# Optimization experiments

Measured on AMD Instinct MI355X. Metric: run time of the kernel, lower is better.

## Reference

```python
import jax, jax.numpy as jnp
import numpy as np

DELTA = 1e-6
B, INPUT, N, WL, R = 32, 1024, 1024, 64, 4
IFACE = WL * R + 3 * WL + 5 * R + 3  # 471


def setup_inputs() -> dict:
    key = jax.random.key(0)
    ks = jax.random.split(key, 9)
    return {
        "x": jax.random.normal(ks[0], (B, INPUT), jnp.float32),
        "W_if": jax.random.normal(ks[1], (INPUT, IFACE), jnp.float32) * 0.02,
        "b_if": jnp.zeros((IFACE,), jnp.float32),
        "memory": jax.random.normal(ks[2], (B, N, WL), jnp.float32) * 0.1,
        "link_matrix": jax.random.uniform(ks[3], (B, 1, N, N), jnp.float32) * 1e-3,
        "precedence": jax.random.uniform(ks[4], (B, 1, N), jnp.float32) * 1e-2,
        "read_weights": jax.random.uniform(ks[5], (B, R, N), jnp.float32) / N,
        "write_weights": jax.random.uniform(ks[6], (B, 1, N), jnp.float32) / N,
        "usage": jax.random.uniform(ks[7], (B, N), jnp.float32),
    }


def _content(memory, keys, strengths):
    # cosine-similarity content addressing; memory [b,N,W], keys [b,h,W]
    mn = memory / (jnp.linalg.norm(memory, axis=-1, keepdims=True) + DELTA)
    kn = keys / (jnp.linalg.norm(keys, axis=-1, keepdims=True) + DELTA)
    sim = jnp.einsum('bhw,bnw->bhn', kn, mn)
    return jax.nn.softmax(sim * strengths[..., None], axis=-1)


def reference(x, W_if, b_if, memory, link_matrix, precedence, read_weights, write_weights, usage):
    b = x.shape[0]
    xi = x @ W_if + b_if  # [b, IFACE]

    # --- parse interface vector (offsets per the torch module) ---
    o = 0
    read_keys = jnp.tanh(xi[:, o:o + R * WL].reshape(b, R, WL)); o += R * WL
    read_strengths = jax.nn.softplus(xi[:, o:o + R]); o += R            # [b,r]
    write_key = jnp.tanh(xi[:, o:o + WL].reshape(b, 1, WL)); o += WL
    write_strength = jax.nn.softplus(xi[:, o:o + 1]); o += 1            # [b,1]
    erase_vector = jax.nn.sigmoid(xi[:, o:o + WL].reshape(b, 1, WL)); o += WL
    write_vector = jnp.tanh(xi[:, o:o + WL].reshape(b, 1, WL)); o += WL
    free_gates = jax.nn.sigmoid(xi[:, o:o + R]); o += R                 # [b,r]
    allocation_gate = jax.nn.sigmoid(xi[:, o:o + 1]); o += 1            # [b,1]
    write_gate = jax.nn.sigmoid(xi[:, o:o + 1]); o += 1                 # [b,1]
    read_modes = jax.nn.softmax(xi[:, o:o + 3 * R].reshape(b, R, 3), axis=-1)

    # --- write phase ---
    wcw = _content(memory, write_key, write_strength)  # [b,1,N]

    # usage update
    u = usage + (1.0 - usage) * (1.0 - jnp.prod(1.0 - write_weights, axis=1))
    psi = jnp.prod(1.0 - free_gates[:, :, None] * read_weights, axis=1)
    u = u * psi

    # allocation via ascending sort + exclusive cumprod, then unsort
    u = DELTA + (1.0 - DELTA) * u
    perm = jnp.argsort(u, axis=1)                       # ascending usage order (phi)
    sorted_u = jnp.take_along_axis(u, perm, axis=1)
    ones_col = jnp.ones((b, 1), u.dtype)
    prod_su = jnp.cumprod(jnp.concatenate([ones_col, sorted_u], axis=1), axis=1)[:, :-1]
    sorted_alloc = (1.0 - sorted_u) * prod_su
    inv_perm = jnp.argsort(perm, axis=1)                # phi_rev: inverse permutation
    alloc = jnp.take_along_axis(sorted_alloc, inv_perm, axis=1)[:, None, :]  # [b,1,N]

    # write weighting
    ag = allocation_gate[..., None]
    wg = write_gate[..., None]
    ww = wg * (ag * alloc + (1.0 - ag) * wcw)           # [b,1,N]

    # memory erase + write (h = 1 write head)
    new_memory = memory * (1.0 - jnp.einsum('bhn,bhw->bnw', ww, erase_vector)) \
                 + jnp.einsum('bhn,bhw->bnw', ww, write_vector)

    # link matrix update (NxN outer-product, zero diagonal)
    ww_i = ww[:, :, :, None]                            # [b,1,N,1]
    ww_j = ww[:, :, None, :]                            # [b,1,1,N]
    prec_j = precedence[:, :, None, :]                  # [b,1,1,N]
    new_link = (1.0 - ww_i - ww_j) * link_matrix + ww_i * prec_j
    eye_mask = 1.0 - jnp.eye(N, dtype=new_link.dtype)
    new_link = new_link * eye_mask[None, None, :, :]

    # precedence update
    new_prec = (1.0 - jnp.sum(ww, axis=-1, keepdims=True)) * precedence + ww

    # --- read phase ---
    fwd_w = jnp.einsum('bhij,brj->bri', new_link, read_weights)   # forward links
    bwd_w = jnp.einsum('bhji,brj->bri', new_link, read_weights)   # backward links
    crw = _content(new_memory, read_keys, read_strengths)         # [b,r,N]
    new_rw = read_modes[..., 0:1] * bwd_w + read_modes[..., 1:2] * crw + read_modes[..., 2:3] * fwd_w
    read_vectors = jnp.einsum('brn,bnw->brw', new_rw, new_memory)  # [b,r,W]
    return read_vectors
```

## Files before the change

### kernel.cpp

```cpp
#include <hip/hip_runtime.h>
#include <math.h>

#define DELTA_ 1e-6f
#define IFACE_ 471
#define XI_STRIDE 480

#define OFF_XI    0
#define OFF_RKN   15360
#define OFF_RS    23552
#define OFF_ER    23680
#define OFF_WV    25728
#define OFF_RM    27776
#define OFF_WW    28160
#define OFF_WWRW  60928
#define OFF_PRD   192000
#define OFF_WRD   192128
#define OFF_INVN  192256
#define OFF_DIAG  225024
#define OFF_NM    257792
#define OFF_RA    2354944
#define OFF_RB    2486016
#define OFF_SAP   2617088
#define OFF_SBP   4714240

__device__ __forceinline__ float sigm_(float x){ return 1.f/(1.f+expf(-x)); }
__device__ __forceinline__ float softp_(float x){ return fmaxf(x,0.f)+log1pf(expf(-fabsf(x))); }
__device__ __forceinline__ float dot4_(float4 a, float4 b){ return a.x*b.x+a.y*b.y+a.z*b.z+a.w*b.w; }

__global__ __launch_bounds__(256) void k_xi(const float* __restrict__ x,
    const float* __restrict__ W, const float* __restrict__ bias,
    float* __restrict__ xi) {
  int b = blockIdx.x;
  int j0 = blockIdx.y*64;
  int t = threadIdx.x;
  int jl = t & 63, kq = t >> 6;
  __shared__ __align__(16) float sx[1024];
  __shared__ float s_part[256];
  for (int q=t; q<256; q+=256) ((float4*)sx)[q] = ((const float4*)(x + b*1024))[q];
  __syncthreads();
  int j = j0 + jl;
  int jc = j < IFACE_ ? j : IFACE_-1;
  float acc = 0.f;
  const float* Wp = W + (size_t)kq*256*IFACE_ + jc;
  #pragma unroll 4
  for (int k=0;k<256;++k) acc += sx[kq*256+k]*Wp[(size_t)k*IFACE_];
  s_part[t] = acc;
  __syncthreads();
  if (t < 64 && (j0+t) < IFACE_) {
    xi[b*XI_STRIDE + j0+t] = s_part[t]+s_part[64+t]+s_part[128+t]+s_part[192+t] + bias[j0+t];
  }
}

__global__ __launch_bounds__(256) void k_batch(
    const float* __restrict__ xi, const float* __restrict__ memory,
    const float* __restrict__ usage, const float* __restrict__ read_w,
    const float* __restrict__ write_w, const float* __restrict__ precedence,
    float* __restrict__ rkn, float* __restrict__ rs, float* __restrict__ er,
    float* __restrict__ wv, float* __restrict__ rm, float* __restrict__ ww_out,
    float* __restrict__ wwrw, float* __restrict__ prd, float* __restrict__ wrd) {
  int b = blockIdx.x; int t = threadIdx.x;
  int lane = t & 63; int wave = t >> 6;
  __shared__ float s_act[472];
  __shared__ __align__(16) float s_key[64];
  __shared__ float s_wcw[1024];
  __shared__ unsigned long long s_k64[1024];
  __shared__ float s_ps[1024];
  __shared__ float s_alloc[1024];
  __shared__ float s_red[32];
  __shared__ float s_bc[2];

  for (int q = t; q < IFACE_; q += 256) {
    float v = xi[b*XI_STRIDE+q];
    float a;
    if      (q < 256) a = tanhf(v);
    else if (q < 260) a = softp_(v);
    else if (q < 324) a = tanhf(v);
    else if (q < 325) a = softp_(v);
    else if (q < 389) a = sigm_(v);
    else if (q < 453) a = tanhf(v);
    else if (q < 459) a = sigm_(v);
    else              a = v;
    s_act[q] = a;
  }
  __syncthreads();
  if (t < 4) {
    float m0=s_act[459+3*t], m1=s_act[460+3*t], m2=s_act[461+3*t];
    float mx=fmaxf(m0,fmaxf(m1,m2));
    float e0=expf(m0-mx), e1=expf(m1-mx), e2=expf(m2-mx);
    float s=e0+e1+e2;
    rm[b*12+3*t+0]=e0/s; rm[b*12+3*t+1]=e1/s; rm[b*12+3*t+2]=e2/s;
  }
  if (t < 64) { er[b*64+t]=s_act[325+t]; wv[b*64+t]=s_act[389+t]; }
  {
    int r = wave;
    float v = s_act[r*64+lane];
    float ss = v*v;
    for (int off=32; off; off>>=1) ss += __shfl_xor(ss, off);
    rkn[((size_t)b*4+r)*64+lane] = v / (sqrtf(ss)+DELTA_);
    if (lane==0) rs[b*4+r] = s_act[256+r];
  }
  if (wave==0) {
    float v = s_act[260+lane];
    float ss=v*v;
    for (int off=32; off; off>>=1) ss += __shfl_xor(ss, off);
    s_key[lane] = v/(sqrtf(ss)+DELTA_);
  }
  __syncthreads();
  float wstr = s_act[324], agv = s_act[457], wgv = s_act[458];

  for (int n=t; n<1024; n+=256) {
    const float4* row = (const float4*)(memory + ((size_t)b*1024+n)*64);
    float dot=0.f, nn2=0.f;
    #pragma unroll
    for (int w4=0; w4<16; ++w4) {
      float4 m4 = row[w4];
      float4 k4 = ((const float4*)s_key)[w4];
      dot += dot4_(m4,k4);
      nn2 += dot4_(m4,m4);
    }
    s_wcw[n] = dot/(sqrtf(nn2)+DELTA_) * wstr;
  }
  __syncthreads();
  {
    float lm=-1e30f;
    for (int n=t;n<1024;n+=256) lm=fmaxf(lm,s_wcw[n]);
    for (int off=32;off;off>>=1) lm=fmaxf(lm,__shfl_xor(lm,off));
    if (lane==0) s_red[wave]=lm;
    __syncthreads();
    if (t==0) s_bc[0]=fmaxf(fmaxf(s_red[0],s_red[1]),fmaxf(s_red[2],s_red[3]));
    __syncthreads();
    float mx=s_bc[0], ls=0.f;
    for (int n=t;n<1024;n+=256){ float e=expf(s_wcw[n]-mx); s_wcw[n]=e; ls+=e; }
    for (int off=32;off;off>>=1) ls+=__shfl_xor(ls,off);
    if (lane==0) s_red[wave]=ls;
    __syncthreads();
    if (t==0) s_bc[1]=s_red[0]+s_red[1]+s_red[2]+s_red[3];
    __syncthreads();
    float inv=1.f/s_bc[1];
    for (int n=t;n<1024;n+=256) s_wcw[n]*=inv;
  }
  __syncthreads();

  for (int n=t; n<1024; n+=256) {
    float us = usage[b*1024+n];
    float wwi = write_w[b*1024+n];
    float u = us + (1.f-us)*wwi;
    float psi = 1.f;
    #pragma unroll
    for (int r=0;r<4;++r) psi *= (1.f - s_act[453+r]*read_w[((size_t)b*4+r)*1024+n]);
    u *= psi;
    u = DELTA_ + (1.f-DELTA_)*u;
    unsigned int ub = __float_as_uint(u);
    s_k64[n] = ((unsigned long long)ub<<32) | (unsigned int)n;
  }

  for (int k=2; k<=1024; k<<=1) {
    for (int j=k>>1; j>0; j>>=1) {
      __syncthreads();
      for (int idx=t; idx<1024; idx+=256) {
        int partner = idx ^ j;
        if (partner > idx) {
          unsigned long long a=s_k64[idx], c=s_k64[partner];
          bool asc = ((idx & k) == 0);
          bool sw = asc ? (a > c) : (a < c);
          if (sw) { s_k64[idx]=c; s_k64[partner]=a; }
        }
      }
    }
  }
  __syncthreads();

  for (int n=t;n<1024;n+=256) s_ps[n] = __uint_as_float((unsigned int)(s_k64[n]>>32));
  __syncthreads();
  for (int off=1; off<1024; off<<=1) {
    float tmp[4];
    #pragma unroll
    for (int m=0;m<4;++m){ int n=t+256*m; tmp[m] = (n>=off)? s_ps[n-off] : 1.f; }
    __syncthreads();
    #pragma unroll
    for (int m=0;m<4;++m){ int n=t+256*m; s_ps[n] *= tmp[m]; }
    __syncthreads();
  }
  for (int n=t;n<1024;n+=256) {
    unsigned long long kv = s_k64[n];
    float su = __uint_as_float((unsigned int)(kv>>32));
    int oi = (int)(kv & 0xffffffffu);
    float prod = (n==0)?1.f:s_ps[n-1];
    s_alloc[oi] = (1.f-su)*prod;
  }
  __syncthreads();

  float pp[4]={0,0,0,0}, wp[4]={0,0,0,0};
  for (int n=t;n<1024;n+=256) {
    float w_ = wgv*(agv*s_alloc[n] + (1.f-agv)*s_wcw[n]);
    ww_out[b*1024+n]=w_;
    float pn = precedence[b*1024+n];
    #pragma unroll
    for (int r=0;r<4;++r){
      float rwv = read_w[((size_t)b*4+r)*1024+n];
      wwrw[((size_t)b*4+r)*1024+n] = w_*rwv;
      pp[r] += pn*rwv;
      wp[r] += w_*rwv;
    }
  }
  #pragma unroll
  for (int r=0;r<4;++r){
    for (int off=32;off;off>>=1){ pp[r]+=__shfl_xor(pp[r],off); wp[r]+=__shfl_xor(wp[r],off); }
  }
  if (lane==0){
    #pragma unroll
    for (int r=0;r<4;++r){ s_red[wave*8+r]=pp[r]; s_red[wave*8+4+r]=wp[r]; }
  }
  __syncthreads();
  if (t<4)              prd[b*4+t]   = s_red[t]+s_red[8+t]+s_red[16+t]+s_red[24+t];
  else if (t<8){ int r=t-4; wrd[b*4+r] = s_red[4+r]+s_red[12+r]+s_red[20+r]+s_red[28+r]; }
}

__global__ __launch_bounds__(256) void k_newmem(const float* __restrict__ memory,
    const float* __restrict__ ww, const float* __restrict__ er,
    const float* __restrict__ wv, float* __restrict__ newmem, float* __restrict__ invn) {
  int b = blockIdx.x;
  int n0 = blockIdx.y*64;
  int t = threadIdx.x;
  int lane16 = t & 15, rl = t >> 4;
  __shared__ float s_ww[64];
  __shared__ __align__(16) float s_er[64];
  __shared__ __align__(16) float s_wv[64];
  if (t < 64) s_ww[t] = ww[b*1024 + n0 + t];
  else if (t < 128) s_er[t-64] = er[b*64 + (t-64)];
  else if (t < 192) s_wv[t-128] = wv[b*64 + (t-128)];
  __syncthreads();
  float4 e4 = ((const float4*)s_er)[lane16];
  float4 v4 = ((const float4*)s_wv)[lane16];
  #pragma unroll
  for (int p=0;p<4;++p) {
    int rloc = p*16 + rl;
    int row = n0 + rloc;
    float wn = s_ww[rloc];
    size_t i4 = ((size_t)b*1024+row)*16 + lane16;
    float4 m4 = ((const float4*)memory)[i4];
    float4 nv;
    nv.x = m4.x*(1.f-wn*e4.x) + wn*v4.x;
    nv.y = m4.y*(1.f-wn*e4.y) + wn*v4.y;
    nv.z = m4.z*(1.f-wn*e4.z) + wn*v4.z;
    nv.w = m4.w*(1.f-wn*e4.w) + wn*v4.w;
    ((float4*)newmem)[i4] = nv;
    float ss = dot4_(nv,nv);
    ss += __shfl_xor(ss,1); ss += __shfl_xor(ss,2);
    ss += __shfl_xor(ss,4); ss += __shfl_xor(ss,8);
    if (lane16==0) invn[b*1024+row] = 1.f/(sqrtf(ss)+DELTA_);
  }
}

__global__ __launch_bounds__(256) void k_fwd(const float* __restrict__ L,
    const float* __restrict__ read_w, const float* __restrict__ wwrw,
    float* __restrict__ RA, float* __restrict__ RB) {
  int b = blockIdx.x;
  int i0 = blockIdx.y*64;
  __shared__ __align__(16) float4 s_rw[4][256];
  __shared__ __align__(16) float4 s_wr[4][256];
  for (int q=threadIdx.x; q<1024; q+=256) {
    int r=q>>8, c4=q&255;
    s_rw[r][c4] = ((const float4*)(read_w + ((size_t)b*4+r)*1024))[c4];
    s_wr[r][c4] = ((const float4*)(wwrw   + ((size_t)b*4+r)*1024))[c4];
  }
  __syncthreads();
  int wave=threadIdx.x>>6, lane=threadIdx.x&63;
  for (int qg=0; qg<4; ++qg) {
    int ib = i0 + wave*16 + qg*4;
    const float4* r0 = (const float4*)(L + ((size_t)b*1024 + ib+0)*1024);
    const float4* r1 = (const float4*)(L + ((size_t)b*1024 + ib+1)*1024);
    const float4* r2 = (const float4*)(L + ((size_t)b*1024 + ib+2)*1024);
    const float4* r3 = (const float4*)(L + ((size_t)b*1024 + ib+3)*1024);
    float acc[4][8];
    #pragma unroll
    for (int q=0;q<4;++q) for (int d=0;d<8;++d) acc[q][d]=0.f;
    #pragma unroll
    for (int m=0;m<4;++m){
      int c4 = lane + (m<<6);
      float4 l0=r0[c4], l1=r1[c4], l2=r2[c4], l3=r3[c4];
      #pragma unroll
      for (int r=0;r<4;++r){
        float4 rv=s_rw[r][c4], wv4=s_wr[r][c4];
        acc[0][r]+=dot4_(l0,rv); acc[0][r+4]+=dot4_(l0,wv4);
        acc[1][r]+=dot4_(l1,rv); acc[1][r+4]+=dot4_(l1,wv4);
        acc[2][r]+=dot4_(l2,rv); acc[2][r+4]+=dot4_(l2,wv4);
        acc[3][r]+=dot4_(l3,rv); acc[3][r+4]+=dot4_(l3,wv4);
      }
    }
    #pragma unroll
    for (int q=0;q<4;++q){
      #pragma unroll
      for (int d=0;d<8;++d){
        float v=acc[q][d];
        for (int off=32;off;off>>=1) v+=__shfl_xor(v,off);
        if (lane==0){
          int i = ib+q;
          if (d<4) RA[((size_t)b*4+d)*1024+i]=v;
          else     RB[((size_t)b*4+(d-4))*1024+i]=v;
        }
      }
    }
  }
}

__global__ __launch_bounds__(256) void k_bwd(const float* __restrict__ L,
    const float* __restrict__ read_w, const float* __restrict__ wwrw,
    float* __restrict__ SAp, float* __restrict__ SBp, float* __restrict__ diag) {
  int b = blockIdx.x;
  int rc = blockIdx.y;
  int i0 = rc*64;
  int t = threadIdx.x;
  __shared__ float s_rw[4][64], s_wr[4][64];
  { int r = t>>6, i = t&63;
    s_rw[r][i]=read_w[((size_t)b*4+r)*1024 + i0+i];
    s_wr[r][i]=wwrw  [((size_t)b*4+r)*1024 + i0+i]; }
  __syncthreads();
  float4 sa0={0,0,0,0},sa1={0,0,0,0},sa2={0,0,0,0},sa3={0,0,0,0};
  float4 sb0={0,0,0,0},sb1={0,0,0,0},sb2={0,0,0,0},sb3={0,0,0,0};
  const float4* Lb = (const float4*)(L + (size_t)b*1048576 + (size_t)i0*1024);
  #pragma unroll 4
  for (int i=0;i<64;++i) {
    float4 lv = Lb[(size_t)i*256 + t];
    float w0=s_rw[0][i], w1=s_rw[1][i], w2=s_rw[2][i], w3=s_rw[3][i];
    float u0=s_wr[0][i], u1=s_wr[1][i], u2=s_wr[2][i], u3=s_wr[3][i];
    sa0.x+=lv.x*w0; sa0.y+=lv.y*w0; sa0.z+=lv.z*w0; sa0.w+=lv.w*w0;
    sa1.x+=lv.x*w1; sa1.y+=lv.y*w1; sa1.z+=lv.z*w1; sa1.w+=lv.w*w1;
    sa2.x+=lv.x*w2; sa2.y+=lv.y*w2; sa2.z+=lv.z*w2; sa2.w+=lv.w*w2;
    sa3.x+=lv.x*w3; sa3.y+=lv.y*w3; sa3.z+=lv.z*w3; sa3.w+=lv.w*w3;
    sb0.x+=lv.x*u0; sb0.y+=lv.y*u0; sb0.z+=lv.z*u0; sb0.w+=lv.w*u0;
    sb1.x+=lv.x*u1; sb1.y+=lv.y*u1; sb1.z+=lv.z*u1; sb1.w+=lv.w*u1;
    sb2.x+=lv.x*u2; sb2.y+=lv.y*u2; sb2.z+=lv.z*u2; sb2.w+=lv.w*u2;
    sb3.x+=lv.x*u3; sb3.y+=lv.y*u3; sb3.z+=lv.z*u3; sb3.w+=lv.w*u3;
    int idx = i0 + i;
    if ((idx>>2) == t) {
      int c = idx & 3;
      float d = (c==0)?lv.x:((c==1)?lv.y:((c==2)?lv.z:lv.w));
      diag[b*1024+idx] = d;
    }
  }
  size_t base = (((size_t)(b*16+rc))*4)*1024;
  ((float4*)(SAp + base          ))[t] = sa0;
  ((float4*)(SAp + base + 1024   ))[t] = sa1;
  ((float4*)(SAp + base + 2048   ))[t] = sa2;
  ((float4*)(SAp + base + 3072   ))[t] = sa3;
  ((float4*)(SBp + base          ))[t] = sb0;
  ((float4*)(SBp + base + 1024   ))[t] = sb1;
  ((float4*)(SBp + base + 2048   ))[t] = sb2;
  ((float4*)(SBp + base + 3072   ))[t] = sb3;
}

__global__ __launch_bounds__(256) void k_read(
    const float* __restrict__ newmem, const float* __restrict__ invn,
    const float* __restrict__ rkn, const float* __restrict__ rs,
    const float* __restrict__ rm, const float* __restrict__ RA,
    const float* __restrict__ RB, const float* __restrict__ SAp,
    const float* __restrict__ SBp, const float* __restrict__ ww,
    const float* __restrict__ precedence, const float* __restrict__ read_w,
    const float* __restrict__ diag, const float* __restrict__ prd,
    const float* __restrict__ wrd, float* __restrict__ out) {
  int b=blockIdx.x, r=blockIdx.y;
  int t=threadIdx.x, lane=t&63, wave=t>>6;
  int lane16 = t & 15, rl = t >> 4;
  __shared__ __align__(16) float s_key[64];
  __shared__ float s_arr[1024];
  __shared__ float s_red[4];
  __shared__ float s_bc[2];
  __shared__ __align__(16) float4 s_acc[16][16];
  if (t<64) s_key[t]=rkn[((size_t)b*4+r)*64+t];
  __syncthreads();
  float rstr = rs[b*4+r];
  float4 key4 = ((const float4*)s_key)[lane16];
  for (int p=0;p<64;++p) {
    int row = p*16 + rl;
    float4 m4 = ((const float4*)newmem)[((size_t)b*1024+row)*16 + lane16];
    float d = dot4_(m4, key4);
    d += __shfl_xor(d,1); d += __shfl_xor(d,2);
    d += __shfl_xor(d,4); d += __shfl_xor(d,8);
    if (lane16==0) s_arr[row] = d * invn[b*1024+row] * rstr;
  }
  __syncthreads();
  {
    float lm=-1e30f;
    for (int n=t;n<1024;n+=256) lm=fmaxf(lm,s_arr[n]);
    for (int off=32;off;off>>=1) lm=fmaxf(lm,__shfl_xor(lm,off));
    if (lane==0) s_red[wave]=lm;
    __syncthreads();
    if (t==0) s_bc[0]=fmaxf(fmaxf(s_red[0],s_red[1]),fmaxf(s_red[2],s_red[3]));
    __syncthreads();
    float mx=s_bc[0], ls=0.f;
    for (int n=t;n<1024;n+=256){ float e=expf(s_arr[n]-mx); s_arr[n]=e; ls+=e; }
    for (int off=32;off;off>>=1) ls+=__shfl_xor(ls,off);
    if (lane==0) s_red[wave]=ls;
    __syncthreads();
    if (t==0) s_bc[1]=s_red[0]+s_red[1]+s_red[2]+s_red[3];
    __syncthreads();
    float inv=1.f/s_bc[1];
    for (int n=t;n<1024;n+=256) s_arr[n]*=inv;
  }
  __syncthreads();
  float m0=rm[b*12+r*3+0], m1=rm[b*12+r*3+1], m2=rm[b*12+r*3+2];
  float pd=prd[b*4+r], wd=wrd[b*4+r];
  for (int n=t;n<1024;n+=256) {
    float ra = RA[((size_t)b*4+r)*1024+n];
    float rb = RB[((size_t)b*4+r)*1024+n];
    float sa=0.f, sb=0.f;
    #pragma unroll
    for (int rc=0;rc<16;++rc){
      sa+=SAp[(((size_t)(b*16+rc))*4+r)*1024+n];
      sb+=SBp[(((size_t)(b*16+rc))*4+r)*1024+n];
    }
    float w_ = ww[b*1024+n];
    float pn = precedence[b*1024+n];
    float rwv= read_w[((size_t)b*4+r)*1024+n];
    float dg = diag[b*1024+n];
    float fwd = (1.f-w_)*ra - rb + w_*pd - ((1.f-2.f*w_)*dg + w_*pn)*rwv;
    float bwd = (1.f-w_)*sa - sb + pn*(wd - w_*rwv) - (1.f-2.f*w_)*dg*rwv;
    float crw = s_arr[n];
    __syncthreads();
    s_arr[n] = m0*bwd + m1*crw + m2*fwd;
    __syncthreads();
  }
  __syncthreads();
  float4 acc = {0,0,0,0};
  for (int p=0;p<64;++p) {
    int row = p*16 + rl;
    float4 m4 = ((const float4*)newmem)[((size_t)b*1024+row)*16 + lane16];
    float s = s_arr[row];
    acc.x += s*m4.x; acc.y += s*m4.y; acc.z += s*m4.z; acc.w += s*m4.w;
  }
  s_acc[rl][lane16] = acc;
  __syncthreads();
  if (t < 16) {
    float4 tot = {0,0,0,0};
    #pragma unroll
    for (int g=0; g<16; ++g) {
      float4 v = s_acc[g][t];
      tot.x+=v.x; tot.y+=v.y; tot.z+=v.z; tot.w+=v.w;
    }
    ((float4*)(out + (b*4+r)*64))[t] = tot;
  }
}

extern "C" void kernel_launch(void* const* d_in, const int* in_sizes, int n_in,
                              void* d_out, int out_size, void* d_ws, size_t ws_size,
                              hipStream_t stream) {
  const float* x      = (const float*)d_in[0];
  const float* W_if   = (const float*)d_in[1];
  const float* b_if   = (const float*)d_in[2];
  const float* memory = (const float*)d_in[3];
  const float* link   = (const float*)d_in[4];
  const float* prec   = (const float*)d_in[5];
  const float* read_w = (const float*)d_in[6];
  const float* write_w= (const float*)d_in[7];
  const float* usage  = (const float*)d_in[8];
  float* out = (float*)d_out;
  float* ws = (float*)d_ws;

  float* xi   = ws + OFF_XI;
  float* rkn  = ws + OFF_RKN;
  float* rs   = ws + OFF_RS;
  float* er   = ws + OFF_ER;
  float* wv   = ws + OFF_WV;
  float* rm   = ws + OFF_RM;
  float* wwp  = ws + OFF_WW;
  float* wwrw = ws + OFF_WWRW;
  float* prd  = ws + OFF_PRD;
  float* wrd  = ws + OFF_WRD;
  float* invn = ws + OFF_INVN;
  float* diag = ws + OFF_DIAG;
  float* nm   = ws + OFF_NM;
  float* RA   = ws + OFF_RA;
  float* RB   = ws + OFF_RB;
  float* SAp  = ws + OFF_SAP;
  float* SBp  = ws + OFF_SBP;

  k_xi<<<dim3(32,8), 256, 0, stream>>>(x, W_if, b_if, xi);
  k_batch<<<dim3(32), 256, 0, stream>>>(xi, memory, usage, read_w, write_w, prec,
                                        rkn, rs, er, wv, rm, wwp, wwrw, prd, wrd);
  k_newmem<<<dim3(32,16), 256, 0, stream>>>(memory, wwp, er, wv, nm, invn);
  k_fwd<<<dim3(32,16), 256, 0, stream>>>(link, read_w, wwrw, RA, RB);
  k_bwd<<<dim3(32,16), 256, 0, stream>>>(link, read_w, wwrw, SAp, SBp, diag);
  k_read<<<dim3(32,4), 256, 0, stream>>>(nm, invn, rkn, rs, rm, RA, RB, SAp, SBp,
                                         wwp, prec, read_w, diag, prd, wrd, out);
}
```

Baseline: 393.2 us.

## Fuse forward and backward link-matrix passes into one tiled scan kernel

Merges the separate forward (row-dot) and backward (column-accumulate) passes over the 128MB link matrix into a single kernel. Each 64x256 tile is loaded once and feeds both products, with forward partials written per column chunk and summed later in k_read. This halves the dominant HBM traffic over the link matrix. In exchange it adds per-row wave shuffle reductions, extra shared-memory staging and a larger partial-sum workspace.

New measurement: 411.4 us. 1.05x slower.

```diff
diff --git a/kernel.cpp b/kernel.cpp
--- a/kernel.cpp
+++ b/kernel.cpp
@@ -18,10 +18,10 @@
 #define OFF_INVN  192256
 #define OFF_DIAG  225024
 #define OFF_NM    257792
-#define OFF_RA    2354944
-#define OFF_RB    2486016
-#define OFF_SAP   2617088
-#define OFF_SBP   4714240
+#define OFF_RAP   2354944
+#define OFF_RBP   2879232
+#define OFF_SAP   3403520
+#define OFF_SBP   5500672
 
 __device__ __forceinline__ float sigm_(float x){ return 1.f/(1.f+expf(-x)); }
 __device__ __forceinline__ float softp_(float x){ return fmaxf(x,0.f)+log1pf(expf(-fabsf(x))); }
@@ -252,109 +252,104 @@
   }
 }
 
-__global__ __launch_bounds__(256) void k_fwd(const float* __restrict__ L,
+__global__ __launch_bounds__(256) void k_scan(const float* __restrict__ L,
     const float* __restrict__ read_w, const float* __restrict__ wwrw,
-    float* __restrict__ RA, float* __restrict__ RB) {
-  int b = blockIdx.x;
-  int i0 = blockIdx.y*64;
-  __shared__ __align__(16) float4 s_rw[4][256];
-  __shared__ __align__(16) float4 s_wr[4][256];
-  for (int q=threadIdx.x; q<1024; q+=256) {
-    int r=q>>8, c4=q&255;
-    s_rw[r][c4] = ((const float4*)(read_w + ((size_t)b*4+r)*1024))[c4];
-    s_wr[r][c4] = ((const float4*)(wwrw   + ((size_t)b*4+r)*1024))[c4];
-  }
-  __syncthreads();
-  int wave=threadIdx.x>>6, lane=threadIdx.x&63;
-  for (int qg=0; qg<4; ++qg) {
-    int ib = i0 + wave*16 + qg*4;
-    const float4* r0 = (const float4*)(L + ((size_t)b*1024 + ib+0)*1024);
-    const float4* r1 = (const float4*)(L + ((size_t)b*1024 + ib+1)*1024);
-    const float4* r2 = (const float4*)(L + ((size_t)b*1024 + ib+2)*1024);
-    const float4* r3 = (const float4*)(L + ((size_t)b*1024 + ib+3)*1024);
-    float acc[4][8];
-    #pragma unroll
-    for (int q=0;q<4;++q) for (int d=0;d<8;++d) acc[q][d]=0.f;
-    #pragma unroll
-    for (int m=0;m<4;++m){
-      int c4 = lane + (m<<6);
-      float4 l0=r0[c4], l1=r1[c4], l2=r2[c4], l3=r3[c4];
-      #pragma unroll
-      for (int r=0;r<4;++r){
-        float4 rv=s_rw[r][c4], wv4=s_wr[r][c4];
-        acc[0][r]+=dot4_(l0,rv); acc[0][r+4]+=dot4_(l0,wv4);
-        acc[1][r]+=dot4_(l1,rv); acc[1][r+4]+=dot4_(l1,wv4);
-        acc[2][r]+=dot4_(l2,rv); acc[2][r+4]+=dot4_(l2,wv4);
-        acc[3][r]+=dot4_(l3,rv); acc[3][r+4]+=dot4_(l3,wv4);
-      }
-    }
-    #pragma unroll
-    for (int q=0;q<4;++q){
-      #pragma unroll
-      for (int d=0;d<8;++d){
-        float v=acc[q][d];
-        for (int off=32;off;off>>=1) v+=__shfl_xor(v,off);
-        if (lane==0){
-          int i = ib+q;
-          if (d<4) RA[((size_t)b*4+d)*1024+i]=v;
-          else     RB[((size_t)b*4+(d-4))*1024+i]=v;
-        }
-      }
-    }
-  }
-}
-
-__global__ __launch_bounds__(256) void k_bwd(const float* __restrict__ L,
-    const float* __restrict__ read_w, const float* __restrict__ wwrw,
-    float* __restrict__ SAp, float* __restrict__ SBp, float* __restrict__ diag) {
-  int b = blockIdx.x;
-  int rc = blockIdx.y;
+    float* __restrict__ RAp, float* __restrict__ RBp,
+    float* __restrict__ SAp, float* __restrict__ SBp,
+    float* __restrict__ diag) {
+  int b = blockIdx.x, rc = blockIdx.y, cc = blockIdx.z;
   int i0 = rc*64;
   int t = threadIdx.x;
-  __shared__ float s_rw[4][64], s_wr[4][64];
-  { int r = t>>6, i = t&63;
-    s_rw[r][i]=read_w[((size_t)b*4+r)*1024 + i0+i];
-    s_wr[r][i]=wwrw  [((size_t)b*4+r)*1024 + i0+i]; }
-  __syncthreads();
-  float4 sa0={0,0,0,0},sa1={0,0,0,0},sa2={0,0,0,0},sa3={0,0,0,0};
-  float4 sb0={0,0,0,0},sb1={0,0,0,0},sb2={0,0,0,0},sb3={0,0,0,0};
-  const float4* Lb = (const float4*)(L + (size_t)b*1048576 + (size_t)i0*1024);
+  int tq = t>>6, tl = t&63;
+  __shared__ __align__(16) float smem[4608];
+  {
+    int r = t>>6, idx = t&63;
+    ((float4*)smem)[r*64+idx]        = ((const float4*)(read_w + ((size_t)b*4+r)*1024 + cc*256))[idx];
+    ((float4*)(smem+1024))[r*64+idx] = ((const float4*)(wwrw   + ((size_t)b*4+r)*1024 + cc*256))[idx];
+    smem[2048 + r*64+idx] = read_w[((size_t)b*4+r)*1024 + i0+idx];
+    smem[2304 + r*64+idx] = wwrw  [((size_t)b*4+r)*1024 + i0+idx];
+  }
+  __syncthreads();
+  float4 sa[4], sb[4];
+  #pragma unroll
+  for (int r=0;r<4;++r){ sa[r]=make_float4(0,0,0,0); sb[r]=make_float4(0,0,0,0); }
+  const float4* L4 = (const float4*)L;
+  size_t base4 = (size_t)b*262144 + (size_t)cc*64 + tl;
+  int dcol4 = cc*64 + tl;
   #pragma unroll 4
-  for (int i=0;i<64;++i) {
-    float4 lv = Lb[(size_t)i*256 + t];
-    float w0=s_rw[0][i], w1=s_rw[1][i], w2=s_rw[2][i], w3=s_rw[3][i];
-    float u0=s_wr[0][i], u1=s_wr[1][i], u2=s_wr[2][i], u3=s_wr[3][i];
-    sa0.x+=lv.x*w0; sa0.y+=lv.y*w0; sa0.z+=lv.z*w0; sa0.w+=lv.w*w0;
-    sa1.x+=lv.x*w1; sa1.y+=lv.y*w1; sa1.z+=lv.z*w1; sa1.w+=lv.w*w1;
-    sa2.x+=lv.x*w2; sa2.y+=lv.y*w2; sa2.z+=lv.z*w2; sa2.w+=lv.w*w2;
-    sa3.x+=lv.x*w3; sa3.y+=lv.y*w3; sa3.z+=lv.z*w3; sa3.w+=lv.w*w3;
-    sb0.x+=lv.x*u0; sb0.y+=lv.y*u0; sb0.z+=lv.z*u0; sb0.w+=lv.w*u0;
-    sb1.x+=lv.x*u1; sb1.y+=lv.y*u1; sb1.z+=lv.z*u1; sb1.w+=lv.w*u1;
-    sb2.x+=lv.x*u2; sb2.y+=lv.y*u2; sb2.z+=lv.z*u2; sb2.w+=lv.w*u2;
-    sb3.x+=lv.x*u3; sb3.y+=lv.y*u3; sb3.z+=lv.z*u3; sb3.w+=lv.w*u3;
-    int idx = i0 + i;
-    if ((idx>>2) == t) {
-      int c = idx & 3;
-      float d = (c==0)?lv.x:((c==1)?lv.y:((c==2)?lv.z:lv.w));
-      diag[b*1024+idx] = d;
-    }
-  }
-  size_t base = (((size_t)(b*16+rc))*4)*1024;
-  ((float4*)(SAp + base          ))[t] = sa0;
-  ((float4*)(SAp + base + 1024   ))[t] = sa1;
-  ((float4*)(SAp + base + 2048   ))[t] = sa2;
-  ((float4*)(SAp + base + 3072   ))[t] = sa3;
-  ((float4*)(SBp + base          ))[t] = sb0;
-  ((float4*)(SBp + base + 1024   ))[t] = sb1;
-  ((float4*)(SBp + base + 2048   ))[t] = sb2;
-  ((float4*)(SBp + base + 3072   ))[t] = sb3;
+  for (int k=0;k<16;++k) {
+    int il = tq*16 + k;
+    int i = i0 + il;
+    float4 lv = L4[base4 + (size_t)i*256];
+    #pragma unroll
+    for (int r=0;r<4;++r) {
+      float wr = smem[2048 + r*64 + il];
+      float ur = smem[2304 + r*64 + il];
+      sa[r].x += lv.x*wr; sa[r].y += lv.y*wr; sa[r].z += lv.z*wr; sa[r].w += lv.w*wr;
+      sb[r].x += lv.x*ur; sb[r].y += lv.y*ur; sb[r].z += lv.z*ur; sb[r].w += lv.w*ur;
+    }
+    if (dcol4 == (i>>2)) {
+      const float* lp = (const float*)&lv;
+      diag[b*1024+i] = lp[i&3];
+    }
+    float pa[4], pb[4];
+    #pragma unroll
+    for (int r=0;r<4;++r) {
+      pa[r] = dot4_(lv, ((const float4*)smem)[r*64+tl]);
+      pb[r] = dot4_(lv, ((const float4*)(smem+1024))[r*64+tl]);
+    }
+    #pragma unroll
+    for (int off=32; off; off>>=1) {
+      #pragma unroll
+      for (int r=0;r<4;++r) { pa[r]+=__shfl_xor(pa[r],off); pb[r]+=__shfl_xor(pb[r],off); }
+    }
+    if (tl==0) {
+      #pragma unroll
+      for (int r=0;r<4;++r) { smem[4096 + r*64 + il] = pa[r]; smem[4096 + (4+r)*64 + il] = pb[r]; }
+    }
+  }
+  __syncthreads();
+  if (t < 64) {
+    #pragma unroll
+    for (int r=0;r<4;++r) {
+      RAp[(((size_t)(b*4+cc))*4+r)*1024 + i0 + t] = smem[4096 + r*64 + t];
+      RBp[(((size_t)(b*4+cc))*4+r)*1024 + i0 + t] = smem[4096 + (4+r)*64 + t];
+    }
+  }
+  #pragma unroll
+  for (int r=0;r<4;++r) ((float4*)smem)[(tq*4+r)*64 + tl] = sa[r];
+  __syncthreads();
+  {
+    int rr = t>>6, cl = t&63;
+    float4 a0 = ((const float4*)smem)[(0*4+rr)*64+cl];
+    float4 a1 = ((const float4*)smem)[(1*4+rr)*64+cl];
+    float4 a2 = ((const float4*)smem)[(2*4+rr)*64+cl];
+    float4 a3 = ((const float4*)smem)[(3*4+rr)*64+cl];
+    float4 tot; tot.x=a0.x+a1.x+a2.x+a3.x; tot.y=a0.y+a1.y+a2.y+a3.y;
+    tot.z=a0.z+a1.z+a2.z+a3.z; tot.w=a0.w+a1.w+a2.w+a3.w;
+    ((float4*)(SAp + (((size_t)(b*16+rc))*4+rr)*1024 + cc*256))[cl] = tot;
+  }
+  __syncthreads();
+  #pragma unroll
+  for (int r=0;r<4;++r) ((float4*)smem)[(tq*4+r)*64 + tl] = sb[r];
+  __syncthreads();
+  {
+    int rr = t>>6, cl = t&63;
+    float4 a0 = ((const float4*)smem)[(0*4+rr)*64+cl];
+    float4 a1 = ((const float4*)smem)[(1*4+rr)*64+cl];
+    float4 a2 = ((const float4*)smem)[(2*4+rr)*64+cl];
+    float4 a3 = ((const float4*)smem)[(3*4+rr)*64+cl];
+    float4 tot; tot.x=a0.x+a1.x+a2.x+a3.x; tot.y=a0.y+a1.y+a2.y+a3.y;
+    tot.z=a0.z+a1.z+a2.z+a3.z; tot.w=a0.w+a1.w+a2.w+a3.w;
+    ((float4*)(SBp + (((size_t)(b*16+rc))*4+rr)*1024 + cc*256))[cl] = tot;
+  }
 }
 
 __global__ __launch_bounds__(256) void k_read(
     const float* __restrict__ newmem, const float* __restrict__ invn,
     const float* __restrict__ rkn, const float* __restrict__ rs,
-    const float* __restrict__ rm, const float* __restrict__ RA,
-    const float* __restrict__ RB, const float* __restrict__ SAp,
+    const float* __restrict__ rm, const float* __restrict__ RAp,
+    const float* __restrict__ RBp, const float* __restrict__ SAp,
     const float* __restrict__ SBp, const float* __restrict__ ww,
     const float* __restrict__ precedence, const float* __restrict__ read_w,
     const float* __restrict__ diag, const float* __restrict__ prd,
@@ -402,8 +397,12 @@
   float m0=rm[b*12+r*3+0], m1=rm[b*12+r*3+1], m2=rm[b*12+r*3+2];
   float pd=prd[b*4+r], wd=wrd[b*4+r];
   for (int n=t;n<1024;n+=256) {
-    float ra = RA[((size_t)b*4+r)*1024+n];
-    float rb = RB[((size_t)b*4+r)*1024+n];
+    float ra=0.f, rb=0.f;
+    #pragma unroll
+    for (int cc=0;cc<4;++cc){
+      ra += RAp[(((size_t)(b*4+cc))*4+r)*1024+n];
+      rb += RBp[(((size_t)(b*4+cc))*4+r)*1024+n];
+    }
     float sa=0.f, sb=0.f;
     #pragma unroll
     for (int rc=0;rc<16;++rc){
@@ -470,8 +469,8 @@
   float* invn = ws + OFF_INVN;
   float* diag = ws + OFF_DIAG;
   float* nm   = ws + OFF_NM;
-  float* RA   = ws + OFF_RA;
-  float* RB   = ws + OFF_RB;
+  float* RAp  = ws + OFF_RAP;
+  float* RBp  = ws + OFF_RBP;
   float* SAp  = ws + OFF_SAP;
   float* SBp  = ws + OFF_SBP;
 
@@ -479,8 +478,7 @@
   k_batch<<<dim3(32), 256, 0, stream>>>(xi, memory, usage, read_w, write_w, prec,
                                         rkn, rs, er, wv, rm, wwp, wwrw, prd, wrd);
   k_newmem<<<dim3(32,16), 256, 0, stream>>>(memory, wwp, er, wv, nm, invn);
-  k_fwd<<<dim3(32,16), 256, 0, stream>>>(link, read_w, wwrw, RA, RB);
-  k_bwd<<<dim3(32,16), 256, 0, stream>>>(link, read_w, wwrw, SAp, SBp, diag);
-  k_read<<<dim3(32,4), 256, 0, stream>>>(nm, invn, rkn, rs, rm, RA, RB, SAp, SBp,
+  k_scan<<<dim3(32,16,4), 256, 0, stream>>>(link, read_w, wwrw, RAp, RBp, SAp, SBp, diag);
+  k_read<<<dim3(32,4), 256, 0, stream>>>(nm, invn, rkn, rs, rm, RAp, RBp, SAp, SBp,
                                          wwp, prec, read_w, diag, prd, wrd, out);
 }
```
